# Kernel tuning notes

Hardware: AMD Instinct MI355X
Metric: run time of the kernel (lower is better)

The kernel has to match this reference:

```python
import jax, jax.numpy as jnp
import numpy as np

N, IN, HID, MAXL, NCLS = 16384, 256, 128, 128, 64
LAYERS, K, EPS = 3, 3, 1e-5

def _gelu(x):
    return jax.nn.gelu(x, approximate=False)  # torch nn.GELU default = exact erf

def _ln(x, w, b):
    # LayerNorm over last axis (torch uses unbiased=False variance)
    m = x.mean(-1, keepdims=True)
    v = ((x - m) ** 2).mean(-1, keepdims=True)
    return (x - m) / jnp.sqrt(v + EPS) * w + b

def setup_inputs() -> dict:
    key = jax.random.key(0)
    ks = jax.random.split(key, 12)
    s = lambda i, shape: jax.random.normal(ks[i], shape, jnp.float32) * 0.02
    return {
        "node_feat": jax.random.normal(ks[0], (N, IN), jnp.float32),
        "neighbor_idx": jax.random.randint(ks[1], (N, MAXL), 0, N, dtype=jnp.int32),
        "neighbor_len": jax.random.randint(ks[2], (N,), 0, MAXL + 1, dtype=jnp.int32),
        "local_W": s(3, (IN, HID)), "local_b": jnp.zeros((HID,), jnp.float32),
        "local_ln_w": jnp.ones((HID,), jnp.float32), "local_ln_b": jnp.zeros((HID,), jnp.float32),
        "ssm_in_W": s(4, (HID, HID)), "ssm_in_b": jnp.zeros((HID,), jnp.float32),
        "conv_w": s(5, (LAYERS, HID, HID, K)), "conv_b": jnp.zeros((LAYERS, HID), jnp.float32),
        "ln_w": jnp.ones((LAYERS, HID), jnp.float32), "ln_b": jnp.zeros((LAYERS, HID), jnp.float32),
        "out_W": s(6, (HID, HID)), "out_b": jnp.zeros((HID,), jnp.float32),
        "cls_W1": s(7, (HID, HID // 2)), "cls_b1": jnp.zeros((HID // 2,), jnp.float32),
        "cls_W2": s(8, (HID // 2, NCLS)), "cls_b2": jnp.zeros((NCLS,), jnp.float32),
    }

def reference(node_feat, neighbor_idx, neighbor_len,
              local_W, local_b, local_ln_w, local_ln_b,
              ssm_in_W, ssm_in_b, conv_w, conv_b, ln_w, ln_b,
              out_W, out_b, cls_W1, cls_b1, cls_W2, cls_b2):
    # local encoder: Linear -> GELU -> LayerNorm over hidden
    H = _ln(_gelu(node_feat @ local_W + local_b), local_ln_w, local_ln_b)  # [N, HID]
    # vectorized ragged gather into padded+masked buffer (replaces per-node python loop)
    mask = jnp.arange(MAXL, dtype=jnp.int32)[None, :] < neighbor_len[:, None]  # [N, MAXL]
    seq = H[neighbor_idx] * mask[..., None]  # [N, MAXL, HID]; padded slots exactly zero
    # SelectiveSSMEncoder
    h = seq @ ssm_in_W + ssm_in_b                 # [N, L, HID]
    h = h.transpose(0, 2, 1)                      # [N, HID, L]
    for i in range(LAYERS):
        d = 2 ** i
        p = (K - 1) * d // 2
        h = jax.lax.conv_general_dilated(
            h, conv_w[i], window_strides=(1,), padding=[(p, p)],
            rhs_dilation=(d,), dimension_numbers=("NCH", "OIH", "NCH"),
        ) + conv_b[i][None, :, None]
        h = _gelu(h)
        # torch LayerNorm(hidden) applied to [N, C, L] normalizes last axis L (== HID here)
        h = _ln(h, ln_w[i], ln_b[i])
    h = h.transpose(0, 2, 1)                      # [N, L, HID]
    out = h @ out_W + out_b                       # [N, L, HID]
    out = out * mask[..., None]
    denom = jnp.maximum(mask.sum(1, keepdims=True).astype(jnp.float32), 1.0)  # [N, 1]
    pooled = out.sum(1) / denom                   # [N, HID]
    logits = _gelu(pooled @ cls_W1 + cls_b1) @ cls_W2 + cls_b2
    return logits
```

## Files before the change

### kernel.cpp

```cpp
#include <hip/hip_runtime.h>
#include <hip/hip_bf16.h>
#include <math.h>

#define NN 16384
#define IN_DIM 256
#define HID 128
#define MAXL 128
#define NCLS 64
#define EPS 1e-5f
#define SROW 144

typedef unsigned short u16;
typedef unsigned int u32;
typedef __attribute__((ext_vector_type(8))) short short8;
typedef __attribute__((ext_vector_type(4))) float f32x4;

#define POOLED 0
#define RSC 128
#define Z1 384

__device__ __forceinline__ u16 f2bf(float f) {
  union { float f; u32 i; } v; v.f = f;
  u32 x = v.i;
  u32 r = (x + 0x7fffu + ((x >> 16) & 1u)) >> 16;
  return (u16)r;
}
#if __has_builtin(__builtin_amdgcn_cvt_pk_bf16_f32)
typedef __bf16 bf16x2 __attribute__((ext_vector_type(2)));
__device__ __forceinline__ u32 pack2(float a, float b) {
  bf16x2 h = __builtin_amdgcn_cvt_pk_bf16_f32(a, b);
  u32 u;
  __builtin_memcpy(&u, &h, 4);
  return u;
}
#else
__device__ __forceinline__ u32 pack2(float a, float b) {
  return (u32)f2bf(a) | ((u32)f2bf(b) << 16);
}
#endif

__device__ __forceinline__ float fast_exp2(float x) {
#if __has_builtin(__builtin_amdgcn_exp2f)
  return __builtin_amdgcn_exp2f(x);
#else
  return exp2f(x);
#endif
}
__device__ __forceinline__ float fast_rcp(float x) {
#if __has_builtin(__builtin_amdgcn_rcpf)
  return __builtin_amdgcn_rcpf(x);
#else
  return 1.0f / x;
#endif
}
__device__ __forceinline__ float gelu_fast(float x) {
  float s = x * x;
  float p = __builtin_fmaf(s, 0.1029445f, 2.3022038f);
  float e = fast_exp2(x * p);
  float r = fast_rcp(e + 1.0f);
  return x - x * r;
}

template <int CTRL>
__device__ __forceinline__ float dpp_add(float x) {
  int y = __builtin_amdgcn_update_dpp(0, __builtin_bit_cast(int, x), CTRL,
                                      0xF, 0xF, true);
  return x + __builtin_bit_cast(float, y);
}
__device__ __forceinline__ float row_reduce16(float x) {
  x = dpp_add<0xB1>(x);
  x = dpp_add<0x4E>(x);
  x = dpp_add<0x124>(x);
  x = dpp_add<0x128>(x);
  return x;
}

__global__ __launch_bounds__(128) void k_local_encoder(
    const float* __restrict__ node_feat, const float* __restrict__ local_W,
    const float* __restrict__ local_b, const float* __restrict__ lnw,
    const float* __restrict__ lnb, u16* __restrict__ H) {
  __shared__ float x[8][IN_DIM];
  __shared__ float red[8][2][2];
  int n0 = blockIdx.x * 8, j = threadIdx.x;
  for (int q = j; q < 8 * IN_DIM; q += 128)
    x[q >> 8][q & 255] = node_feat[n0 * IN_DIM + q];
  __syncthreads();
  float acc[8];
#pragma unroll
  for (int p = 0; p < 8; ++p) acc[p] = local_b[j];
  for (int k = 0; k < IN_DIM; ++k) {
    float w = local_W[k * HID + j];
#pragma unroll
    for (int p = 0; p < 8; ++p) acc[p] += x[p][k] * w;
  }
  float lw = lnw[j], lb = lnb[j];
  int wave = j >> 6;
  float g[8];
#pragma unroll
  for (int p = 0; p < 8; ++p) {
    g[p] = gelu_fast(acc[p]);
    float s = g[p], ss = g[p] * g[p];
#pragma unroll
    for (int o = 1; o < 64; o <<= 1) {
      s += __shfl_xor(s, o, 64);
      ss += __shfl_xor(ss, o, 64);
    }
    if ((j & 63) == 0) { red[p][wave][0] = s; red[p][wave][1] = ss; }
  }
  __syncthreads();
#pragma unroll
  for (int p = 0; p < 8; ++p) {
    float S = red[p][0][0] + red[p][1][0];
    float SS = red[p][0][1] + red[p][1][1];
    float m = S * (1.0f / 128.0f);
    float v = SS * (1.0f / 128.0f) - m * m;
    float y = (g[p] - m) * rsqrtf(v + EPS) * lw + lb;
    H[(n0 + p) * HID + j] = f2bf(y);
  }
}

#define CONV_ELEMS (3 * 4 * 3 * 8 * 512)
#define PREP_TOTAL (CONV_ELEMS + 2 * HID * HID)
__global__ __launch_bounds__(256) void k_prep(
    const float* __restrict__ conv_w, const float* __restrict__ ssm_W,
    const float* __restrict__ out_W, u16* __restrict__ dst) {
  int idx = blockIdx.x * 256 + threadIdx.x;
  if (idx >= PREP_TOTAL) return;
  if (idx < CONV_ELEMS) {
    int e = idx & 7, quad = (idx >> 3) & 3, li16 = (idx >> 5) & 15,
        g = (idx >> 9) & 7;
    int rest = idx >> 12;
    int tap = rest % 3, kcli = rest / 3;
    int kc = kcli & 3, li = kcli >> 2;
    int co = g * 16 + li16, ci = kc * 32 + quad * 8 + e;
    dst[idx] = f2bf(conv_w[((li * HID + co) * HID + ci) * 3 + tap]);
  } else {
    int r = idx - CONV_ELEMS;
    int sel = r >> 14;
    r &= 16383;
    int e = r & 7, quad = (r >> 3) & 3, li16 = (r >> 5) & 15, g = (r >> 9) & 7;
    int kc = r >> 12;
    const float* src = sel ? out_W : ssm_W;
    dst[idx] = f2bf(src[(kc * 32 + quad * 8 + e) * HID + g * 16 + li16]);
  }
}

template <int TAPS, int DIL>
__device__ __forceinline__ void run_gemm(f32x4 (*acc)[8],
                                         const u16* __restrict__ Wg,
                                         const u16* __restrict__ Sin, int li16,
                                         int quad, int w) {
  const u16* wbase = Wg + w * 1024 + li16 * 32 + quad * 8;
#pragma unroll
  for (int kc = 0; kc < 4; ++kc) {
#pragma unroll
    for (int tap = 0; tap < TAPS; ++tap) {
      const int shift = (TAPS == 3) ? (tap - 1) * DIL : 0;
      const u16* wp = wbase + (kc * TAPS + tap) * 4096;
      short8 a0 = *(const short8*)wp;
      short8 a1 = *(const short8*)(wp + 512);
      int base_row = 4 + li16 + shift;
      int phys = (kc * 4 + quad) ^ (base_row & 7);
      const u16* sp = Sin + base_row * SROW + phys * 8;
#pragma unroll
      for (int j0 = 0; j0 < 8; j0 += 4) {
        short8 b[4];
#pragma unroll
        for (int jj = 0; jj < 4; ++jj)
          b[jj] = *(const short8*)(sp + (j0 + jj) * 16 * SROW);
#pragma unroll
        for (int jj = 0; jj < 4; ++jj) {
          acc[0][j0 + jj] = __builtin_amdgcn_mfma_f32_16x16x32_bf16(
              a0, b[jj], acc[0][j0 + jj], 0, 0, 0);
          acc[1][j0 + jj] = __builtin_amdgcn_mfma_f32_16x16x32_bf16(
              a1, b[jj], acc[1][j0 + jj], 0, 0, 0);
        }
      }
    }
  }
}

__device__ __forceinline__ void bias_acc(f32x4 (*acc)[8],
                                         const float* __restrict__ cb,
                                         int cobase, int quad) {
#pragma unroll
  for (int i = 0; i < 2; ++i) {
    f32x4 b4 = *(const f32x4*)(cb + cobase + i * 16 + quad * 4);
#pragma unroll
    for (int j = 0; j < 8; ++j) acc[i][j] = b4;
  }
}

__device__ __forceinline__ void store_pk(const uint2 (*pk)[8],
                                         u16* __restrict__ S, int li16,
                                         int quad, int w) {
#pragma unroll
  for (int i = 0; i < 2; ++i) {
    int c8 = w * 4 + 2 * i + (quad >> 1);
#pragma unroll
    for (int j = 0; j < 8; ++j) {
      int row = 4 + 16 * j + li16;
      int phys = c8 ^ (row & 7);
      *(uint2*)&S[row * SROW + phys * 8 + (quad & 1) * 4] = pk[i][j];
    }
  }
}

template <int DIL>
__device__ __forceinline__ void conv_stage(
    f32x4 (*acc)[8], const u16* __restrict__ Wg, u16* __restrict__ S,
    int li16, int quad, int w, const float* __restrict__ cb,
    const float* __restrict__ gw, const float* __restrict__ gb) {
  int cobase = w * 32;
  bias_acc(acc, cb, cobase, quad);
  run_gemm<3, DIL>(acc, Wg, S, li16, quad, w);
  float gl[8], bl[8];
#pragma unroll
  for (int j = 0; j < 8; ++j) {
    int l = 16 * j + li16;
    gl[j] = gw[l];
    bl[j] = gb[l];
  }
  uint2 pk[2][8];
#pragma unroll
  for (int i = 0; i < 2; ++i) {
    f32x4 s = (f32x4){0.f, 0.f, 0.f, 0.f}, ss = s;
#pragma unroll
    for (int j = 0; j < 8; ++j) {
#pragma unroll
      for (int r = 0; r < 4; ++r) acc[i][j][r] = gelu_fast(acc[i][j][r]);
      s += acc[i][j];
      ss += acc[i][j] * acc[i][j];
    }
#pragma unroll
    for (int r = 0; r < 4; ++r) {
      s[r] = row_reduce16(s[r]);
      ss[r] = row_reduce16(ss[r]);
    }
    f32x4 inv, im;
#pragma unroll
    for (int r = 0; r < 4; ++r) {
      float m = s[r] * (1.0f / 128.0f);
      float var = ss[r] * (1.0f / 128.0f) - m * m;
      inv[r] = rsqrtf(var + EPS);
      im[r] = m * inv[r];
    }
#pragma unroll
    for (int j = 0; j < 8; ++j) {
      float y0 = __builtin_fmaf(__builtin_fmaf(acc[i][j][0], inv[0], -im[0]), gl[j], bl[j]);
      float y1 = __builtin_fmaf(__builtin_fmaf(acc[i][j][1], inv[1], -im[1]), gl[j], bl[j]);
      float y2 = __builtin_fmaf(__builtin_fmaf(acc[i][j][2], inv[2], -im[2]), gl[j], bl[j]);
      float y3 = __builtin_fmaf(__builtin_fmaf(acc[i][j][3], inv[3], -im[3]), gl[j], bl[j]);
      pk[i][j].x = pack2(y0, y1);
      pk[i][j].y = pack2(y2, y3);
    }
  }
  __syncthreads();
  store_pk(pk, S, li16, quad, w);
  __syncthreads();
}

__global__ __launch_bounds__(256, 3) void k_main(
    const int* __restrict__ nidx, const int* __restrict__ nlen,
    const u16* __restrict__ Hg, const u16* __restrict__ ssmW3,
    const float* __restrict__ ssm_b, const u16* __restrict__ convW3,
    const float* __restrict__ conv_b, const float* __restrict__ lnw,
    const float* __restrict__ lnb, const u16* __restrict__ outW3,
    const float* __restrict__ out_b, const float* __restrict__ W1,
    const float* __restrict__ b1, const float* __restrict__ W2,
    const float* __restrict__ b2, float* __restrict__ out) {
  __shared__ __align__(16) u16 S[136 * SROW];
  float* scr = (float*)S;

  int n = blockIdx.x, t = threadIdx.x;
  int lane = t & 63, w = t >> 6;
  int li16 = lane & 15, quad = lane >> 4;
  int len = nlen[n];

  if (t < 128) {
    int rg = t >> 4, c = t & 15;
    int row = (rg < 4) ? rg : 128 + rg;
    uint4 z; z.x = 0; z.y = 0; z.z = 0; z.w = 0;
    *(uint4*)&S[row * SROW + c * 8] = z;
  }
  {
    int l = t >> 1, h = t & 1;
    int nb = nidx[n * MAXL + l];
    bool valid = l < len;
    const uint4* Hrow = (const uint4*)(Hg + nb * HID + h * 64);
    int row = 4 + l;
    int rx = row & 7;
#pragma unroll
    for (int mb = 0; mb < 8; ++mb) {
      uint4 v = Hrow[mb];
      if (!valid) { v.x = 0; v.y = 0; v.z = 0; v.w = 0; }
      int phys = (h * 8 + mb) ^ rx;
      *(uint4*)&S[row * SROW + phys * 8] = v;
    }
  }
  __syncthreads();

  f32x4 acc[2][8];
  int cobase = w * 32;

  bias_acc(acc, ssm_b, cobase, quad);
  run_gemm<1, 0>(acc, ssmW3, S, li16, quad, w);
  {
    uint2 pk[2][8];
#pragma unroll
    for (int i = 0; i < 2; ++i) {
#pragma unroll
      for (int j = 0; j < 8; ++j) {
        pk[i][j].x = pack2(acc[i][j][0], acc[i][j][1]);
        pk[i][j].y = pack2(acc[i][j][2], acc[i][j][3]);
      }
    }
    __syncthreads();
    store_pk(pk, S, li16, quad, w);
    __syncthreads();
  }

  conv_stage<1>(acc, convW3, S, li16, quad, w, conv_b, lnw, lnb);
  conv_stage<2>(acc, convW3 + 49152, S, li16, quad, w, conv_b + HID,
                lnw + HID, lnb + HID);
  conv_stage<4>(acc, convW3 + 98304, S, li16, quad, w, conv_b + 2 * HID,
                lnw + 2 * HID, lnb + 2 * HID);

  bias_acc(acc, out_b, cobase, quad);
  run_gemm<1, 0>(acc, outW3, S, li16, quad, w);
  f32x4 pf[2];
  {
    float denom = (len > 0) ? (float)len : 1.0f;
#pragma unroll
    for (int i = 0; i < 2; ++i) {
      f32x4 s = (f32x4){0.f, 0.f, 0.f, 0.f};
#pragma unroll
      for (int j = 0; j < 8; ++j) {
        int l = 16 * j + li16;
        if (l < len) s += acc[i][j];
      }
#pragma unroll
      for (int r = 0; r < 4; ++r) {
        float sv = row_reduce16(s[r]);
        pf[i][r] = (len > 0) ? (sv / denom) : 0.f;
      }
    }
  }
  __syncthreads();
  if (li16 == 0) {
#pragma unroll
    for (int i = 0; i < 2; ++i)
      *(f32x4*)&scr[POOLED + cobase + 16 * i + quad * 4] = pf[i];
  }
  __syncthreads();
  {
    int part = t >> 6, j = t & 63;
    float s = 0.f;
    int c0 = part * 32;
#pragma unroll 8
    for (int c = c0; c < c0 + 32; ++c) s += scr[POOLED + c] * W1[c * 64 + j];
    scr[RSC + part * 64 + j] = s;
  }
  __syncthreads();
  if (t < 64) {
    float z = b1[t] + scr[RSC + t] + scr[RSC + 64 + t] + scr[RSC + 128 + t] +
              scr[RSC + 192 + t];
    scr[Z1 + t] = gelu_fast(z);
  }
  __syncthreads();
  {
    int part = t >> 6, j = t & 63;
    float s = 0.f;
    int c0 = part * 16;
#pragma unroll 8
    for (int c = c0; c < c0 + 16; ++c) s += scr[Z1 + c] * W2[c * 64 + j];
    scr[RSC + part * 64 + j] = s;
  }
  __syncthreads();
  if (t < 64) {
    out[n * NCLS + t] = b2[t] + scr[RSC + t] + scr[RSC + 64 + t] +
                        scr[RSC + 128 + t] + scr[RSC + 192 + t];
  }
}

extern "C" void kernel_launch(void* const* d_in, const int* in_sizes, int n_in,
                              void* d_out, int out_size, void* d_ws,
                              size_t ws_size, hipStream_t stream) {
  const float* node_feat = (const float*)d_in[0];
  const int* nidx = (const int*)d_in[1];
  const int* nlen = (const int*)d_in[2];
  const float* local_W = (const float*)d_in[3];
  const float* local_b = (const float*)d_in[4];
  const float* local_ln_w = (const float*)d_in[5];
  const float* local_ln_b = (const float*)d_in[6];
  const float* ssm_W = (const float*)d_in[7];
  const float* ssm_b = (const float*)d_in[8];
  const float* conv_w = (const float*)d_in[9];
  const float* conv_b = (const float*)d_in[10];
  const float* lnw = (const float*)d_in[11];
  const float* lnb = (const float*)d_in[12];
  const float* outW = (const float*)d_in[13];
  const float* outb = (const float*)d_in[14];
  const float* W1 = (const float*)d_in[15];
  const float* b1 = (const float*)d_in[16];
  const float* W2 = (const float*)d_in[17];
  const float* b2 = (const float*)d_in[18];

  u16* Hws = (u16*)d_ws;
  u16* convW3 = Hws + NN * HID;
  u16* ssmW3 = convW3 + CONV_ELEMS;
  u16* outW3 = ssmW3 + HID * HID;

  k_local_encoder<<<NN / 8, 128, 0, stream>>>(node_feat, local_W, local_b,
                                              local_ln_w, local_ln_b, Hws);
  k_prep<<<(PREP_TOTAL + 255) / 256, 256, 0, stream>>>(conv_w, ssm_W, outW,
                                                       convW3);
  k_main<<<NN, 256, 0, stream>>>(nidx, nlen, Hws, ssmW3, ssm_b, convW3, conv_b,
                                 lnw, lnb, outW3, outb, W1, b1, W2, b2,
                                 (float*)d_out);
}
```

Before: 994.8 us.

## Split GEMM accumulators into two half-sequence passes to raise occupancy

```diff
diff --git a/kernel.cpp b/kernel.cpp
--- a/kernel.cpp
+++ b/kernel.cpp
@@ -38,6 +38,12 @@
   return (u32)f2bf(a) | ((u32)f2bf(b) << 16);
 }
 #endif
+__device__ __forceinline__ float bflo(u32 p) {
+  return __builtin_bit_cast(float, p << 16);
+}
+__device__ __forceinline__ float bfhi(u32 p) {
+  return __builtin_bit_cast(float, p & 0xffff0000u);
+}
 
 __device__ __forceinline__ float fast_exp2(float x) {
 #if __has_builtin(__builtin_amdgcn_exp2f)
@@ -145,11 +151,11 @@
   }
 }
 
-template <int TAPS, int DIL>
-__device__ __forceinline__ void run_gemm(f32x4 (*acc)[8],
-                                         const u16* __restrict__ Wg,
-                                         const u16* __restrict__ Sin, int li16,
-                                         int quad, int w) {
+template <int TAPS, int DIL, int J0>
+__device__ __forceinline__ void run_gemm4(f32x4 (*acc)[4],
+                                          const u16* __restrict__ Wg,
+                                          const u16* __restrict__ Sin,
+                                          int li16, int quad, int w) {
   const u16* wbase = Wg + w * 1024 + li16 * 32 + quad * 8;
 #pragma unroll
   for (int kc = 0; kc < 4; ++kc) {
@@ -161,33 +167,30 @@
       short8 a1 = *(const short8*)(wp + 512);
       int base_row = 4 + li16 + shift;
       int phys = (kc * 4 + quad) ^ (base_row & 7);
-      const u16* sp = Sin + base_row * SROW + phys * 8;
-#pragma unroll
-      for (int j0 = 0; j0 < 8; j0 += 4) {
-        short8 b[4];
-#pragma unroll
-        for (int jj = 0; jj < 4; ++jj)
-          b[jj] = *(const short8*)(sp + (j0 + jj) * 16 * SROW);
-#pragma unroll
-        for (int jj = 0; jj < 4; ++jj) {
-          acc[0][j0 + jj] = __builtin_amdgcn_mfma_f32_16x16x32_bf16(
-              a0, b[jj], acc[0][j0 + jj], 0, 0, 0);
-          acc[1][j0 + jj] = __builtin_amdgcn_mfma_f32_16x16x32_bf16(
-              a1, b[jj], acc[1][j0 + jj], 0, 0, 0);
-        }
-      }
-    }
-  }
-}
-
-__device__ __forceinline__ void bias_acc(f32x4 (*acc)[8],
-                                         const float* __restrict__ cb,
-                                         int cobase, int quad) {
+      const u16* sp = Sin + (base_row + 16 * J0) * SROW + phys * 8;
+      short8 b[4];
+#pragma unroll
+      for (int jj = 0; jj < 4; ++jj)
+        b[jj] = *(const short8*)(sp + jj * 16 * SROW);
+#pragma unroll
+      for (int jj = 0; jj < 4; ++jj) {
+        acc[0][jj] = __builtin_amdgcn_mfma_f32_16x16x32_bf16(a0, b[jj],
+                                                             acc[0][jj], 0, 0, 0);
+        acc[1][jj] = __builtin_amdgcn_mfma_f32_16x16x32_bf16(a1, b[jj],
+                                                             acc[1][jj], 0, 0, 0);
+      }
+    }
+  }
+}
+
+__device__ __forceinline__ void bias_acc4(f32x4 (*acc)[4],
+                                          const float* __restrict__ cb,
+                                          int cobase, int quad) {
 #pragma unroll
   for (int i = 0; i < 2; ++i) {
     f32x4 b4 = *(const f32x4*)(cb + cobase + i * 16 + quad * 4);
 #pragma unroll
-    for (int j = 0; j < 8; ++j) acc[i][j] = b4;
+    for (int j = 0; j < 4; ++j) acc[i][j] = b4;
   }
 }
 
@@ -208,12 +211,45 @@
 
 template <int DIL>
 __device__ __forceinline__ void conv_stage(
-    f32x4 (*acc)[8], const u16* __restrict__ Wg, u16* __restrict__ S,
-    int li16, int quad, int w, const float* __restrict__ cb,
-    const float* __restrict__ gw, const float* __restrict__ gb) {
+    const u16* __restrict__ Wg, u16* __restrict__ S, int li16, int quad,
+    int w, const float* __restrict__ cb, const float* __restrict__ gw,
+    const float* __restrict__ gb) {
   int cobase = w * 32;
-  bias_acc(acc, cb, cobase, quad);
-  run_gemm<3, DIL>(acc, Wg, S, li16, quad, w);
+  f32x4 sum[2], sq[2];
+#pragma unroll
+  for (int i = 0; i < 2; ++i) {
+    sum[i] = (f32x4){0.f, 0.f, 0.f, 0.f};
+    sq[i] = (f32x4){0.f, 0.f, 0.f, 0.f};
+  }
+  uint2 pk[2][8];
+  f32x4 acc[2][4];
+
+  bias_acc4(acc, cb, cobase, quad);
+  run_gemm4<3, DIL, 0>(acc, Wg, S, li16, quad, w);
+#pragma unroll
+  for (int i = 0; i < 2; ++i)
+#pragma unroll
+    for (int j = 0; j < 4; ++j) {
+#pragma unroll
+      for (int r = 0; r < 4; ++r) acc[i][j][r] = gelu_fast(acc[i][j][r]);
+      sum[i] += acc[i][j];
+      sq[i] += acc[i][j] * acc[i][j];
+      pk[i][j].x = pack2(acc[i][j][0], acc[i][j][1]);
+      pk[i][j].y = pack2(acc[i][j][2], acc[i][j][3]);
+    }
+
+  bias_acc4(acc, cb, cobase, quad);
+  run_gemm4<3, DIL, 4>(acc, Wg, S, li16, quad, w);
+#pragma unroll
+  for (int i = 0; i < 2; ++i)
+#pragma unroll
+    for (int j = 0; j < 4; ++j) {
+#pragma unroll
+      for (int r = 0; r < 4; ++r) acc[i][j][r] = gelu_fast(acc[i][j][r]);
+      sum[i] += acc[i][j];
+      sq[i] += acc[i][j] * acc[i][j];
+    }
+
   float gl[8], bl[8];
 #pragma unroll
   for (int j = 0; j < 8; ++j) {
@@ -221,36 +257,35 @@
     gl[j] = gw[l];
     bl[j] = gb[l];
   }
-  uint2 pk[2][8];
 #pragma unroll
   for (int i = 0; i < 2; ++i) {
-    f32x4 s = (f32x4){0.f, 0.f, 0.f, 0.f}, ss = s;
-#pragma unroll
-    for (int j = 0; j < 8; ++j) {
-#pragma unroll
-      for (int r = 0; r < 4; ++r) acc[i][j][r] = gelu_fast(acc[i][j][r]);
-      s += acc[i][j];
-      ss += acc[i][j] * acc[i][j];
-    }
+    f32x4 inv, im;
 #pragma unroll
     for (int r = 0; r < 4; ++r) {
-      s[r] = row_reduce16(s[r]);
-      ss[r] = row_reduce16(ss[r]);
-    }
-    f32x4 inv, im;
-#pragma unroll
-    for (int r = 0; r < 4; ++r) {
-      float m = s[r] * (1.0f / 128.0f);
-      float var = ss[r] * (1.0f / 128.0f) - m * m;
+      float sv = row_reduce16(sum[i][r]);
+      float qv = row_reduce16(sq[i][r]);
+      float m = sv * (1.0f / 128.0f);
+      float var = qv * (1.0f / 128.0f) - m * m;
       inv[r] = rsqrtf(var + EPS);
       im[r] = m * inv[r];
     }
 #pragma unroll
-    for (int j = 0; j < 8; ++j) {
-      float y0 = __builtin_fmaf(__builtin_fmaf(acc[i][j][0], inv[0], -im[0]), gl[j], bl[j]);
-      float y1 = __builtin_fmaf(__builtin_fmaf(acc[i][j][1], inv[1], -im[1]), gl[j], bl[j]);
-      float y2 = __builtin_fmaf(__builtin_fmaf(acc[i][j][2], inv[2], -im[2]), gl[j], bl[j]);
-      float y3 = __builtin_fmaf(__builtin_fmaf(acc[i][j][3], inv[3], -im[3]), gl[j], bl[j]);
+    for (int j = 0; j < 4; ++j) {
+      float y0 = __builtin_fmaf(__builtin_fmaf(acc[i][j][0], inv[0], -im[0]), gl[4 + j], bl[4 + j]);
+      float y1 = __builtin_fmaf(__builtin_fmaf(acc[i][j][1], inv[1], -im[1]), gl[4 + j], bl[4 + j]);
+      float y2 = __builtin_fmaf(__builtin_fmaf(acc[i][j][2], inv[2], -im[2]), gl[4 + j], bl[4 + j]);
+      float y3 = __builtin_fmaf(__builtin_fmaf(acc[i][j][3], inv[3], -im[3]), gl[4 + j], bl[4 + j]);
+      pk[i][4 + j].x = pack2(y0, y1);
+      pk[i][4 + j].y = pack2(y2, y3);
+    }
+#pragma unroll
+    for (int j = 0; j < 4; ++j) {
+      float x0 = bflo(pk[i][j].x), x1 = bfhi(pk[i][j].x);
+      float x2 = bflo(pk[i][j].y), x3 = bfhi(pk[i][j].y);
+      float y0 = __builtin_fmaf(__builtin_fmaf(x0, inv[0], -im[0]), gl[j], bl[j]);
+      float y1 = __builtin_fmaf(__builtin_fmaf(x1, inv[1], -im[1]), gl[j], bl[j]);
+      float y2 = __builtin_fmaf(__builtin_fmaf(x2, inv[2], -im[2]), gl[j], bl[j]);
+      float y3 = __builtin_fmaf(__builtin_fmaf(x3, inv[3], -im[3]), gl[j], bl[j]);
       pk[i][j].x = pack2(y0, y1);
       pk[i][j].y = pack2(y2, y3);
     }
@@ -260,7 +295,7 @@
   __syncthreads();
 }
 
-__global__ __launch_bounds__(256, 3) void k_main(
+__global__ __launch_bounds__(256, 4) void k_main(
     const int* __restrict__ nidx, const int* __restrict__ nlen,
     const u16* __restrict__ Hg, const u16* __restrict__ ssmW3,
     const float* __restrict__ ssm_b, const u16* __restrict__ convW3,
@@ -300,51 +335,72 @@
   }
   __syncthreads();
 
-  f32x4 acc[2][8];
   int cobase = w * 32;
 
-  bias_acc(acc, ssm_b, cobase, quad);
-  run_gemm<1, 0>(acc, ssmW3, S, li16, quad, w);
   {
     uint2 pk[2][8];
-#pragma unroll
-    for (int i = 0; i < 2; ++i) {
-#pragma unroll
-      for (int j = 0; j < 8; ++j) {
+    f32x4 acc[2][4];
+    bias_acc4(acc, ssm_b, cobase, quad);
+    run_gemm4<1, 0, 0>(acc, ssmW3, S, li16, quad, w);
+#pragma unroll
+    for (int i = 0; i < 2; ++i)
+#pragma unroll
+      for (int j = 0; j < 4; ++j) {
         pk[i][j].x = pack2(acc[i][j][0], acc[i][j][1]);
         pk[i][j].y = pack2(acc[i][j][2], acc[i][j][3]);
       }
-    }
+    bias_acc4(acc, ssm_b, cobase, quad);
+    run_gemm4<1, 0, 4>(acc, ssmW3, S, li16, quad, w);
+#pragma unroll
+    for (int i = 0; i < 2; ++i)
+#pragma unroll
+      for (int j = 0; j < 4; ++j) {
+        pk[i][4 + j].x = pack2(acc[i][j][0], acc[i][j][1]);
+        pk[i][4 + j].y = pack2(acc[i][j][2], acc[i][j][3]);
+      }
     __syncthreads();
     store_pk(pk, S, li16, quad, w);
     __syncthreads();
   }
 
-  conv_stage<1>(acc, convW3, S, li16, quad, w, conv_b, lnw, lnb);
-  conv_stage<2>(acc, convW3 + 49152, S, li16, quad, w, conv_b + HID,
+  conv_stage<1>(convW3, S, li16, quad, w, conv_b, lnw, lnb);
+  conv_stage<2>(convW3 + 49152, S, li16, quad, w, conv_b + HID,
                 lnw + HID, lnb + HID);
-  conv_stage<4>(acc, convW3 + 98304, S, li16, quad, w, conv_b + 2 * HID,
+  conv_stage<4>(convW3 + 98304, S, li16, quad, w, conv_b + 2 * HID,
                 lnw + 2 * HID, lnb + 2 * HID);
 
-  bias_acc(acc, out_b, cobase, quad);
-  run_gemm<1, 0>(acc, outW3, S, li16, quad, w);
   f32x4 pf[2];
   {
+    f32x4 ps[2];
+    ps[0] = (f32x4){0.f, 0.f, 0.f, 0.f};
+    ps[1] = (f32x4){0.f, 0.f, 0.f, 0.f};
+    f32x4 acc[2][4];
+    bias_acc4(acc, out_b, cobase, quad);
+    run_gemm4<1, 0, 0>(acc, outW3, S, li16, quad, w);
+#pragma unroll
+    for (int i = 0; i < 2; ++i)
+#pragma unroll
+      for (int j = 0; j < 4; ++j) {
+        int l = 16 * j + li16;
+        if (l < len) ps[i] += acc[i][j];
+      }
+    bias_acc4(acc, out_b, cobase, quad);
+    run_gemm4<1, 0, 4>(acc, outW3, S, li16, quad, w);
+#pragma unroll
+    for (int i = 0; i < 2; ++i)
+#pragma unroll
+      for (int j = 0; j < 4; ++j) {
+        int l = 16 * (4 + j) + li16;
+        if (l < len) ps[i] += acc[i][j];
+      }
     float denom = (len > 0) ? (float)len : 1.0f;
 #pragma unroll
-    for (int i = 0; i < 2; ++i) {
-      f32x4 s = (f32x4){0.f, 0.f, 0.f, 0.f};
-#pragma unroll
-      for (int j = 0; j < 8; ++j) {
-        int l = 16 * j + li16;
-        if (l < len) s += acc[i][j];
-      }
+    for (int i = 0; i < 2; ++i)
 #pragma unroll
       for (int r = 0; r < 4; ++r) {
-        float sv = row_reduce16(s[r]);
+        float sv = row_reduce16(ps[i][r]);
         pf[i][r] = (len > 0) ? (sv / denom) : 0.f;
       }
-    }
   }
   __syncthreads();
   if (li16 == 0) {
```

Measured after the change: 1.011 ms. Within noise of the previous version (+1.6%).

## Hoist SSM input projection per node and pool before output projection

Applied to the files above, without the earlier changes.

```diff
diff --git a/kernel.cpp b/kernel.cpp
--- a/kernel.cpp
+++ b/kernel.cpp
@@ -38,6 +38,12 @@
   return (u32)f2bf(a) | ((u32)f2bf(b) << 16);
 }
 #endif
+__device__ __forceinline__ float bflo(u32 p) {
+  return __builtin_bit_cast(float, p << 16);
+}
+__device__ __forceinline__ float bfhi(u32 p) {
+  return __builtin_bit_cast(float, p & 0xffff0000u);
+}
 
 __device__ __forceinline__ float fast_exp2(float x) {
 #if __has_builtin(__builtin_amdgcn_exp2f)
@@ -120,10 +126,10 @@
 }
 
 #define CONV_ELEMS (3 * 4 * 3 * 8 * 512)
-#define PREP_TOTAL (CONV_ELEMS + 2 * HID * HID)
+#define PREP_TOTAL (CONV_ELEMS + HID * HID + HID)
 __global__ __launch_bounds__(256) void k_prep(
     const float* __restrict__ conv_w, const float* __restrict__ ssm_W,
-    const float* __restrict__ out_W, u16* __restrict__ dst) {
+    const float* __restrict__ ssm_b, u16* __restrict__ dst) {
   int idx = blockIdx.x * 256 + threadIdx.x;
   if (idx >= PREP_TOTAL) return;
   if (idx < CONV_ELEMS) {
@@ -134,14 +140,13 @@
     int kc = kcli & 3, li = kcli >> 2;
     int co = g * 16 + li16, ci = kc * 32 + quad * 8 + e;
     dst[idx] = f2bf(conv_w[((li * HID + co) * HID + ci) * 3 + tap]);
-  } else {
+  } else if (idx < CONV_ELEMS + HID * HID) {
     int r = idx - CONV_ELEMS;
-    int sel = r >> 14;
-    r &= 16383;
     int e = r & 7, quad = (r >> 3) & 3, li16 = (r >> 5) & 15, g = (r >> 9) & 7;
     int kc = r >> 12;
-    const float* src = sel ? out_W : ssm_W;
-    dst[idx] = f2bf(src[(kc * 32 + quad * 8 + e) * HID + g * 16 + li16]);
+    dst[idx] = f2bf(ssm_W[(kc * 32 + quad * 8 + e) * HID + g * 16 + li16]);
+  } else {
+    dst[idx] = f2bf(ssm_b[idx - CONV_ELEMS - HID * HID]);
   }
 }
 
@@ -202,6 +207,45 @@
       int row = 4 + 16 * j + li16;
       int phys = c8 ^ (row & 7);
       *(uint2*)&S[row * SROW + phys * 8 + (quad & 1) * 4] = pk[i][j];
+    }
+  }
+}
+
+__global__ __launch_bounds__(256) void k_ssm(const float* __restrict__ ssm_b,
+                                             const u16* __restrict__ ssmW3,
+                                             u16* __restrict__ H) {
+  __shared__ __align__(16) u16 S[136 * SROW];
+  int t = threadIdx.x;
+  int lane = t & 63, w = t >> 6;
+  int li16 = lane & 15, quad = lane >> 4;
+  int n0 = blockIdx.x * 128;
+  {
+    int l = t >> 1, h = t & 1;
+    const uint4* Hrow = (const uint4*)(H + (n0 + l) * HID + h * 64);
+    int row = 4 + l, rx = row & 7;
+#pragma unroll
+    for (int mb = 0; mb < 8; ++mb) {
+      uint4 v = Hrow[mb];
+      int phys = (h * 8 + mb) ^ rx;
+      *(uint4*)&S[row * SROW + phys * 8] = v;
+    }
+  }
+  __syncthreads();
+  f32x4 acc[2][8];
+  int cobase = w * 32;
+  bias_acc(acc, ssm_b, cobase, quad);
+  run_gemm<1, 0>(acc, ssmW3, S, li16, quad, w);
+  u32* H2 = (u32*)H;
+#pragma unroll
+  for (int i = 0; i < 2; ++i) {
+    int co0 = cobase + i * 16 + quad * 4;
+#pragma unroll
+    for (int j = 0; j < 8; ++j) {
+      int node = n0 + 16 * j + li16;
+      uint2 pk;
+      pk.x = pack2(acc[i][j][0], acc[i][j][1]);
+      pk.y = pack2(acc[i][j][2], acc[i][j][3]);
+      *(uint2*)&H2[node * 64 + co0 / 2] = pk;
     }
   }
 }
@@ -262,15 +306,16 @@
 
 __global__ __launch_bounds__(256, 3) void k_main(
     const int* __restrict__ nidx, const int* __restrict__ nlen,
-    const u16* __restrict__ Hg, const u16* __restrict__ ssmW3,
-    const float* __restrict__ ssm_b, const u16* __restrict__ convW3,
-    const float* __restrict__ conv_b, const float* __restrict__ lnw,
-    const float* __restrict__ lnb, const u16* __restrict__ outW3,
-    const float* __restrict__ out_b, const float* __restrict__ W1,
-    const float* __restrict__ b1, const float* __restrict__ W2,
-    const float* __restrict__ b2, float* __restrict__ out) {
+    const u16* __restrict__ Hg, const u16* __restrict__ biasrow,
+    const u16* __restrict__ convW3, const float* __restrict__ conv_b,
+    const float* __restrict__ lnw, const float* __restrict__ lnb,
+    const float* __restrict__ out_W, const float* __restrict__ out_b,
+    const float* __restrict__ W1, const float* __restrict__ b1,
+    const float* __restrict__ W2, const float* __restrict__ b2,
+    float* __restrict__ out) {
   __shared__ __align__(16) u16 S[136 * SROW];
   float* scr = (float*)S;
+  float* csum = (float*)&S[132 * SROW];
 
   int n = blockIdx.x, t = threadIdx.x;
   int lane = t & 63, w = t >> 6;
@@ -283,17 +328,22 @@
     uint4 z; z.x = 0; z.y = 0; z.z = 0; z.w = 0;
     *(uint4*)&S[row * SROW + c * 8] = z;
   }
+  if (t < 16) {
+    int rg = t >> 1, half = t & 1;
+    int row = (rg < 4) ? rg : 128 + rg;
+    uint4 z; z.x = 0; z.y = 0; z.z = 0; z.w = 0;
+    *(uint4*)&S[row * SROW + 128 + half * 8] = z;
+  }
   {
     int l = t >> 1, h = t & 1;
     int nb = nidx[n * MAXL + l];
     bool valid = l < len;
-    const uint4* Hrow = (const uint4*)(Hg + nb * HID + h * 64);
-    int row = 4 + l;
-    int rx = row & 7;
+    const uint4* src = valid ? (const uint4*)(Hg + nb * HID + h * 64)
+                             : (const uint4*)(biasrow + h * 64);
+    int row = 4 + l, rx = row & 7;
 #pragma unroll
     for (int mb = 0; mb < 8; ++mb) {
-      uint4 v = Hrow[mb];
-      if (!valid) { v.x = 0; v.y = 0; v.z = 0; v.w = 0; }
+      uint4 v = src[mb];
       int phys = (h * 8 + mb) ^ rx;
       *(uint4*)&S[row * SROW + phys * 8] = v;
     }
@@ -301,24 +351,6 @@
   __syncthreads();
 
   f32x4 acc[2][8];
-  int cobase = w * 32;
-
-  bias_acc(acc, ssm_b, cobase, quad);
-  run_gemm<1, 0>(acc, ssmW3, S, li16, quad, w);
-  {
-    uint2 pk[2][8];
-#pragma unroll
-    for (int i = 0; i < 2; ++i) {
-#pragma unroll
-      for (int j = 0; j < 8; ++j) {
-        pk[i][j].x = pack2(acc[i][j][0], acc[i][j][1]);
-        pk[i][j].y = pack2(acc[i][j][2], acc[i][j][3]);
-      }
-    }
-    __syncthreads();
-    store_pk(pk, S, li16, quad, w);
-    __syncthreads();
-  }
 
   conv_stage<1>(acc, convW3, S, li16, quad, w, conv_b, lnw, lnb);
   conv_stage<2>(acc, convW3 + 49152, S, li16, quad, w, conv_b + HID,
@@ -326,31 +358,47 @@
   conv_stage<4>(acc, convW3 + 98304, S, li16, quad, w, conv_b + 2 * HID,
                 lnw + 2 * HID, lnb + 2 * HID);
 
-  bias_acc(acc, out_b, cobase, quad);
-  run_gemm<1, 0>(acc, outW3, S, li16, quad, w);
-  f32x4 pf[2];
-  {
+  {
+    int q = t & 31, g = t >> 5;
+    int c8 = q >> 1, off = (q & 1) * 4;
+    float cs0 = 0.f, cs1 = 0.f, cs2 = 0.f, cs3 = 0.f;
+#pragma unroll
+    for (int k = 0; k < 16; ++k) {
+      int l = g * 16 + k;
+      int row = 4 + l;
+      int phys = c8 ^ (row & 7);
+      uint2 v = *(const uint2*)&S[row * SROW + phys * 8 + off];
+      if (l >= len) { v.x = 0; v.y = 0; }
+      cs0 += bflo(v.x); cs1 += bfhi(v.x);
+      cs2 += bflo(v.y); cs3 += bfhi(v.y);
+    }
+    cs0 += __shfl_xor(cs0, 32, 64);
+    cs1 += __shfl_xor(cs1, 32, 64);
+    cs2 += __shfl_xor(cs2, 32, 64);
+    cs3 += __shfl_xor(cs3, 32, 64);
+    if (lane < 32) {
+      atomicAdd(&csum[q * 4 + 0], cs0);
+      atomicAdd(&csum[q * 4 + 1], cs1);
+      atomicAdd(&csum[q * 4 + 2], cs2);
+      atomicAdd(&csum[q * 4 + 3], cs3);
+    }
+  }
+  __syncthreads();
+  {
+    int co = t & 127, part = t >> 7;
+    const float* wcol = out_W + co;
+    float a = 0.f;
+    int ci0 = part * 64;
+#pragma unroll 8
+    for (int ci = ci0; ci < ci0 + 64; ++ci)
+      a = __builtin_fmaf(csum[ci], wcol[ci * HID], a);
+    scr[RSC + part * 128 + co] = a;
+  }
+  __syncthreads();
+  if (t < 128) {
     float denom = (len > 0) ? (float)len : 1.0f;
-#pragma unroll
-    for (int i = 0; i < 2; ++i) {
-      f32x4 s = (f32x4){0.f, 0.f, 0.f, 0.f};
-#pragma unroll
-      for (int j = 0; j < 8; ++j) {
-        int l = 16 * j + li16;
-        if (l < len) s += acc[i][j];
-      }
-#pragma unroll
-      for (int r = 0; r < 4; ++r) {
-        float sv = row_reduce16(s[r]);
-        pf[i][r] = (len > 0) ? (sv / denom) : 0.f;
-      }
-    }
-  }
-  __syncthreads();
-  if (li16 == 0) {
-#pragma unroll
-    for (int i = 0; i < 2; ++i)
-      *(f32x4*)&scr[POOLED + cobase + 16 * i + quad * 4] = pf[i];
+    float p = (scr[RSC + t] + scr[RSC + 128 + t]) / denom;
+    scr[POOLED + t] = (len > 0) ? (p + out_b[t]) : 0.f;
   }
   __syncthreads();
   {
@@ -409,13 +457,14 @@
   u16* Hws = (u16*)d_ws;
   u16* convW3 = Hws + NN * HID;
   u16* ssmW3 = convW3 + CONV_ELEMS;
-  u16* outW3 = ssmW3 + HID * HID;
+  u16* biasrow = ssmW3 + HID * HID;
 
   k_local_encoder<<<NN / 8, 128, 0, stream>>>(node_feat, local_W, local_b,
                                               local_ln_w, local_ln_b, Hws);
-  k_prep<<<(PREP_TOTAL + 255) / 256, 256, 0, stream>>>(conv_w, ssm_W, outW,
+  k_prep<<<(PREP_TOTAL + 255) / 256, 256, 0, stream>>>(conv_w, ssm_W, ssm_b,
                                                        convW3);
-  k_main<<<NN, 256, 0, stream>>>(nidx, nlen, Hws, ssmW3, ssm_b, convW3, conv_b,
-                                 lnw, lnb, outW3, outb, W1, b1, W2, b2,
+  k_ssm<<<NN / 128, 256, 0, stream>>>(ssm_b, ssmW3, Hws);
+  k_main<<<NN, 256, 0, stream>>>(nidx, nlen, Hws, biasrow, convW3, conv_b,
+                                 lnw, lnb, outW, outb, W1, b1, W2, b2,
                                  (float*)d_out);
 }
```

New measurement: 879.2 us. 11.6% less time.
